# Performance work log

Measured on AMD Instinct MI355X. Metric: run time of the kernel, lower is better.

Reference implementation:

```python
import jax, jax.numpy as jnp
import numpy as np

IN_DIM = 128
HID = 128
OUT = 1
N_USER = 100000
N_ITEM = 50000
E = 1000000


def _mlp_params(key, in_dim, hid, out):
    k0, k1, k2 = jax.random.split(key, 3)
    s0 = float(np.sqrt(2.0 / in_dim))
    s1 = float(np.sqrt(2.0 / hid))
    return dict(
        W0=jax.random.normal(k0, (in_dim, hid), jnp.float32) * s0,
        b0=jnp.zeros((hid,), jnp.float32),
        W1=jax.random.normal(k1, (hid, hid), jnp.float32) * s1,
        b1=jnp.zeros((hid,), jnp.float32),
        W2=jax.random.normal(k2, (hid, out), jnp.float32) * s1,
        b2=jnp.zeros((out,), jnp.float32),
    )


def setup_inputs() -> dict:
    key = jax.random.key(0)
    ks = jax.random.split(key, 8)
    inp = {
        "user_emb": jax.random.normal(ks[0], (N_USER, IN_DIM), jnp.float32),
        "item_emb": jax.random.normal(ks[1], (N_ITEM, IN_DIM), jnp.float32),
        "ui_src": jax.random.randint(ks[2], (E,), 0, N_USER, jnp.int64),
        "ui_dst": jax.random.randint(ks[3], (E,), 0, N_ITEM, jnp.int64),
        "iu_src": jax.random.randint(ks[4], (E,), 0, N_ITEM, jnp.int64),
        "iu_dst": jax.random.randint(ks[5], (E,), 0, N_USER, jnp.int64),
    }
    for name, k in (("ui", ks[6]), ("iu", ks[7])):
        p = _mlp_params(k, 2 * IN_DIM, HID, OUT)
        for pn, pv in p.items():
            inp[f"{pn}_{name}"] = pv
    return inp


def _decode(src_emb, dst_emb, src_idx, dst_idx, W0, b0, W1, b1, W2, b2):
    # gather + concat -> [E, 2*in_dim]
    e = jnp.concatenate([src_emb[src_idx], dst_emb[dst_idx]], axis=1)
    h = jax.nn.elu(e @ W0 + b0)   # bilinear layer + ELU
    h = jax.nn.elu(h @ W1 + b1)   # linear1 + ELU
    return jax.nn.sigmoid(h @ W2 + b2).reshape(-1)  # linear2 + sigmoid, [E]


def reference(user_emb, item_emb, ui_src, ui_dst, iu_src, iu_dst,
              W0_ui, b0_ui, W1_ui, b1_ui, W2_ui, b2_ui,
              W0_iu, b0_iu, W1_iu, b1_iu, W2_iu, b2_iu):
    p_ui = _decode(user_emb, item_emb, ui_src, ui_dst,
                   W0_ui, b0_ui, W1_ui, b1_ui, W2_ui, b2_ui)
    p_iu = _decode(item_emb, user_emb, iu_src, iu_dst,
                   W0_iu, b0_iu, W1_iu, b1_iu, W2_iu, b2_iu)
    return p_ui, p_iu
```

## Files before the change

kernel.cpp:

```cpp
#include <hip/hip_runtime.h>
#include <cstdint>
#include <cstddef>


#define E_EDGES       1000000
#define NTILES        31250
#define GRID_BLKS     512
#define WAVES_PER_DEC 2048

typedef _Float16 half8  __attribute__((ext_vector_type(8)));
typedef _Float16 half4v __attribute__((ext_vector_type(4)));
typedef _Float16 half2v __attribute__((ext_vector_type(2)));
typedef float    f32x4  __attribute__((ext_vector_type(4)));
typedef unsigned int uint4v __attribute__((ext_vector_type(4)));

__device__ __forceinline__ float elu_f(float x) {
    return (x > 0.f) ? x : (__expf(x) - 1.f);
}

__device__ __forceinline__ void mfma_a(f32x4& acc, half8 af, half8 bf) {
    asm("v_mfma_f32_16x16x32_f16 %0, %1, %2, %0"
        : "+a"(acc)
        : "v"(af), "v"(bf));
}

__device__ __forceinline__ void xpose_pair(unsigned int A0, unsigned int A1,
                                           unsigned int& lo, unsigned int& hi) {
#if __has_builtin(__builtin_amdgcn_permlane32_swap) && __has_builtin(__builtin_amdgcn_permlane16_swap)
    auto t = __builtin_amdgcn_permlane32_swap(A0, A1, false, false);
    auto u = __builtin_amdgcn_permlane16_swap(t[0], t[1], false, false);
    lo = u[0]; hi = u[1];
#else
    const int l = (int)(threadIdx.x & 63);
    const int src = (((l >> 4) & 1) << 5) | (l & 15);
    unsigned int x0 = (unsigned int)__shfl((int)A0, src);
    unsigned int x1 = (unsigned int)__shfl((int)A1, src);
    unsigned int y0 = (unsigned int)__shfl((int)A0, src + 16);
    unsigned int y1 = (unsigned int)__shfl((int)A1, src + 16);
    lo = (l < 32) ? x0 : x1;
    hi = (l < 32) ? y0 : y1;
#endif
}

__global__ void cvt_tables(const float* __restrict__ u, const float* __restrict__ it,
                           _Float16* __restrict__ ou, _Float16* __restrict__ oi,
                           int n4u, int n4i) {
    int i = blockIdx.x * blockDim.x + threadIdx.x;
    const float4* src; half4v* dst; int j;
    if (i < n4u) { src = (const float4*)u; dst = (half4v*)ou; j = i; }
    else {
        j = i - n4u;
        if (j >= n4i) return;
        src = (const float4*)it; dst = (half4v*)oi;
    }
    float4 f = src[j];
    half4v h;
    h[0] = (_Float16)f.x; h[1] = (_Float16)f.y;
    h[2] = (_Float16)f.z; h[3] = (_Float16)f.w;
    dst[j] = h;
}

template<bool PRE16>
__global__ __launch_bounds__(512, 2) void edge_mlp(
    const void* __restrict__ tabU, const void* __restrict__ tabI,
    const int* __restrict__ ui_src, const int* __restrict__ ui_dst,
    const int* __restrict__ iu_src, const int* __restrict__ iu_dst,
    const float* __restrict__ W0_ui, const float* __restrict__ b0_ui,
    const float* __restrict__ W1_ui, const float* __restrict__ b1_ui,
    const float* __restrict__ W2_ui, const float* __restrict__ b2_ui,
    const float* __restrict__ W0_iu, const float* __restrict__ b0_iu,
    const float* __restrict__ W1_iu, const float* __restrict__ b1_iu,
    const float* __restrict__ W2_iu, const float* __restrict__ b2_iu,
    float* __restrict__ out)
{
    __shared__ __align__(16) _Float16 wlds[49152];

    const int dec = blockIdx.x & 1;
    const void* src_tab = dec ? tabI : tabU;
    const void* dst_tab = dec ? tabU : tabI;
    const int* src_idx = dec ? iu_src : ui_src;
    const int* dst_idx = dec ? iu_dst : ui_dst;
    const float* W0 = dec ? W0_iu : W0_ui;
    const float* b0 = dec ? b0_iu : b0_ui;
    const float* W1 = dec ? W1_iu : W1_ui;
    const float* b1 = dec ? b1_iu : b1_ui;
    const float* W2 = dec ? W2_iu : W2_ui;
    const float* b2 = dec ? b2_iu : b2_ui;
    float* op = out + (dec ? E_EDGES : 0);

    const int tid = threadIdx.x;
    const int l = tid & 63;
    const int w = tid >> 6;
    const int n = l & 15;
    const int g = l >> 4;

    #pragma unroll
    for (int q = 0; q < 8; ++q) {
        const int f = w * 8 + q;
        const int kk = f >> 3, hr = f & 7;
        const int kbase = kk * 32 + g * 8;
        const int col = hr * 16 + n;
        half8 fr;
        #pragma unroll
        for (int i = 0; i < 8; ++i) fr[i] = (_Float16)W0[(kbase + i) * 128 + col];
        *(half8*)&wlds[f * 512 + l * 8] = fr;
    }
    #pragma unroll
    for (int q = 0; q < 4; ++q) {
        const int f = w * 4 + q;
        const int kk = f >> 3, hr = f & 7;
        const int kbase = kk * 32 + g * 8;
        const int col = hr * 16 + n;
        half8 fr;
        #pragma unroll
        for (int i = 0; i < 8; ++i) fr[i] = (_Float16)W1[(kbase + i) * 128 + col];
        *(half8*)&wlds[32768 + f * 512 + l * 8] = fr;
    }

    f32x4 b0r[8], b1r[8], w2r[8];
    #pragma unroll
    for (int hr = 0; hr < 8; ++hr) {
        b0r[hr] = *(const f32x4*)&b0[hr * 16 + g * 4];
        b1r[hr] = *(const f32x4*)&b1[hr * 16 + g * 4];
        w2r[hr] = *(const f32x4*)&W2[hr * 16 + g * 4];
    }
    const float b2s = b2[0];
    __syncthreads();

    const half8* w0f = (const half8*)&wlds[0];
    const half8* w1f = (const half8*)&wlds[32768];

    const int wid = (blockIdx.x >> 1) * 8 + w;

    for (int t = wid; t < NTILES; t += WAVES_PER_DEC) {
        const int e0 = t * 32;

        half8 a[2][8];
        #pragma unroll
        for (int s = 0; s < 2; ++s) {
            const int e = e0 + s * 16 + n;
            const int si = src_idx[e];
            const int di = dst_idx[e];
            if constexpr (PRE16) {
                const half8* rs = (const half8*)((const _Float16*)src_tab + (size_t)si * 128) + g;
                const half8* rd = (const half8*)((const _Float16*)dst_tab + (size_t)di * 128) + g;
                #pragma unroll
                for (int kk = 0; kk < 4; ++kk) a[s][kk]     = rs[kk * 4];
                #pragma unroll
                for (int kk = 0; kk < 4; ++kk) a[s][4 + kk] = rd[kk * 4];
            } else {
                const float* rs = (const float*)src_tab + (size_t)si * 128 + g * 8;
                const float* rd = (const float*)dst_tab + (size_t)di * 128 + g * 8;
                #pragma unroll
                for (int kk = 0; kk < 8; ++kk) {
                    const float* base = (kk < 4) ? (rs + kk * 32) : (rd + (kk - 4) * 32);
                    float4 p0 = *(const float4*)base;
                    float4 p1 = *(const float4*)(base + 4);
                    half8 fr;
                    fr[0] = (_Float16)p0.x; fr[1] = (_Float16)p0.y;
                    fr[2] = (_Float16)p0.z; fr[3] = (_Float16)p0.w;
                    fr[4] = (_Float16)p1.x; fr[5] = (_Float16)p1.y;
                    fr[6] = (_Float16)p1.z; fr[7] = (_Float16)p1.w;
                    a[s][kk] = fr;
                }
            }
        }

        f32x4 acc0[2][8];
        #pragma unroll
        for (int s = 0; s < 2; ++s)
            #pragma unroll
            for (int hr = 0; hr < 8; ++hr) acc0[s][hr] = (f32x4){0.f, 0.f, 0.f, 0.f};
        #pragma unroll
        for (int kk = 0; kk < 8; ++kk) {
            #pragma unroll
            for (int hr = 0; hr < 8; ++hr) {
                const half8 wf = w0f[(kk * 8 + hr) * 64 + l];
                mfma_a(acc0[0][hr], wf, a[0][kk]);
                mfma_a(acc0[1][hr], wf, a[1][kk]);
            }
        }

        unsigned int v01[2][8], v23[2][8];
        #pragma unroll
        for (int hr = 0; hr < 8; ++hr) {
            #pragma unroll
            for (int s = 0; s < 2; ++s) {
                half2v p01, p23;
                p01[0] = (_Float16)elu_f(acc0[s][hr][0] + b0r[hr][0]);
                p01[1] = (_Float16)elu_f(acc0[s][hr][1] + b0r[hr][1]);
                p23[0] = (_Float16)elu_f(acc0[s][hr][2] + b0r[hr][2]);
                p23[1] = (_Float16)elu_f(acc0[s][hr][3] + b0r[hr][3]);
                v01[s][hr] = __builtin_bit_cast(unsigned int, p01);
                v23[s][hr] = __builtin_bit_cast(unsigned int, p23);
            }
        }
        half8 bfr[2][4];
        #pragma unroll
        for (int s = 0; s < 2; ++s) {
            #pragma unroll
            for (int kk = 0; kk < 4; ++kk) {
                unsigned int w0lo, w0hi, w1lo, w1hi;
                xpose_pair(v01[s][2 * kk], v01[s][2 * kk + 1], w0lo, w0hi);
                xpose_pair(v23[s][2 * kk], v23[s][2 * kk + 1], w1lo, w1hi);
                uint4v wd;
                wd.x = w0lo;
                wd.y = w1lo;
                wd.z = w0hi;
                wd.w = w1hi;
                bfr[s][kk] = __builtin_bit_cast(half8, wd);
            }
        }

        f32x4 acc1[2][8];
        #pragma unroll
        for (int s = 0; s < 2; ++s)
            #pragma unroll
            for (int hr = 0; hr < 8; ++hr) acc1[s][hr] = (f32x4){0.f, 0.f, 0.f, 0.f};
        #pragma unroll
        for (int kk = 0; kk < 4; ++kk) {
            #pragma unroll
            for (int hr = 0; hr < 8; ++hr) {
                const half8 wf = w1f[(kk * 8 + hr) * 64 + l];
                mfma_a(acc1[0][hr], wf, bfr[0][kk]);
                mfma_a(acc1[1][hr], wf, bfr[1][kk]);
            }
        }

        float accs0 = 0.f, accs1 = 0.f;
        #pragma unroll
        for (int hr = 0; hr < 8; ++hr) {
            #pragma unroll
            for (int v = 0; v < 4; ++v) {
                accs0 += elu_f(acc1[0][hr][v] + b1r[hr][v]) * w2r[hr][v];
                accs1 += elu_f(acc1[1][hr][v] + b1r[hr][v]) * w2r[hr][v];
            }
        }
        accs0 += __shfl_xor(accs0, 16); accs0 += __shfl_xor(accs0, 32);
        accs1 += __shfl_xor(accs1, 16); accs1 += __shfl_xor(accs1, 32);
        if (l < 32) {
            const float sel = (l & 16) ? accs1 : accs0;
            op[e0 + l] = 1.f / (1.f + __expf(-(sel + b2s)));
        }
    }
}

extern "C" void kernel_launch(void* const* d_in, const int* in_sizes, int n_in,
                              void* d_out, int out_size, void* d_ws, size_t ws_size,
                              hipStream_t stream) {
    const float* user_emb = (const float*)d_in[0];
    const float* item_emb = (const float*)d_in[1];
    const int* ui_src = (const int*)d_in[2];
    const int* ui_dst = (const int*)d_in[3];
    const int* iu_src = (const int*)d_in[4];
    const int* iu_dst = (const int*)d_in[5];
    const float* W0_ui = (const float*)d_in[6];
    const float* b0_ui = (const float*)d_in[7];
    const float* W1_ui = (const float*)d_in[8];
    const float* b1_ui = (const float*)d_in[9];
    const float* W2_ui = (const float*)d_in[10];
    const float* b2_ui = (const float*)d_in[11];
    const float* W0_iu = (const float*)d_in[12];
    const float* b0_iu = (const float*)d_in[13];
    const float* W1_iu = (const float*)d_in[14];
    const float* b1_iu = (const float*)d_in[15];
    const float* W2_iu = (const float*)d_in[16];
    const float* b2_iu = (const float*)d_in[17];
    float* out = (float*)d_out;

    const size_t nuser = (size_t)100000 * 128;
    const size_t nitem = (size_t)50000 * 128;
    const size_t need = (nuser + nitem) * sizeof(unsigned short);

    if (ws_size >= need) {
        _Float16* u16 = (_Float16*)d_ws;
        _Float16* i16 = u16 + nuser;
        const int n4u = (int)(nuser / 4);
        const int n4i = (int)(nitem / 4);
        cvt_tables<<<dim3((unsigned)((n4u + n4i + 255) / 256)), dim3(256), 0, stream>>>(
            user_emb, item_emb, u16, i16, n4u, n4i);
        edge_mlp<true><<<dim3(GRID_BLKS), dim3(512), 0, stream>>>(
            (const void*)u16, (const void*)i16,
            ui_src, ui_dst, iu_src, iu_dst,
            W0_ui, b0_ui, W1_ui, b1_ui, W2_ui, b2_ui,
            W0_iu, b0_iu, W1_iu, b1_iu, W2_iu, b2_iu, out);
    } else {
        edge_mlp<false><<<dim3(GRID_BLKS), dim3(512), 0, stream>>>(
            (const void*)user_emb, (const void*)item_emb,
            ui_src, ui_dst, iu_src, iu_dst,
            W0_ui, b0_ui, W1_ui, b1_ui, W2_ui, b2_ui,
            W0_iu, b0_iu, W1_iu, b1_iu, W2_iu, b2_iu, out);
    }
}
```

Measured before the change: 422.7 us.

## Software-pipeline embedding gathers and index loads across tiles in edge MLP loop

```diff
diff --git a/kernel.cpp b/kernel.cpp
--- a/kernel.cpp
+++ b/kernel.cpp
@@ -10,12 +10,15 @@
 
 typedef _Float16 half8  __attribute__((ext_vector_type(8)));
 typedef _Float16 half4v __attribute__((ext_vector_type(4)));
-typedef _Float16 half2v __attribute__((ext_vector_type(2)));
 typedef float    f32x4  __attribute__((ext_vector_type(4)));
 typedef unsigned int uint4v __attribute__((ext_vector_type(4)));
 
 __device__ __forceinline__ float elu_f(float x) {
     return (x > 0.f) ? x : (__expf(x) - 1.f);
+}
+
+__device__ __forceinline__ unsigned int pk16(float lo, float hi) {
+    return __builtin_bit_cast(unsigned int, __builtin_amdgcn_cvt_pkrtz(lo, hi));
 }
 
 __device__ __forceinline__ void mfma_a(f32x4& acc, half8 af, half8 bf) {
@@ -61,6 +64,51 @@
 }
 
 template<bool PRE16>
+__device__ __forceinline__ void gather_tiles(
+    half8 (&a)[2][8], const void* src_tab, const void* dst_tab,
+    const int (&si)[2], const int (&di)[2], int g)
+{
+    #pragma unroll
+    for (int s = 0; s < 2; ++s) {
+        if constexpr (PRE16) {
+            const half8* rs = (const half8*)((const _Float16*)src_tab + (size_t)si[s] * 128) + g;
+            const half8* rd = (const half8*)((const _Float16*)dst_tab + (size_t)di[s] * 128) + g;
+            #pragma unroll
+            for (int kk = 0; kk < 4; ++kk) a[s][kk]     = rs[kk * 4];
+            #pragma unroll
+            for (int kk = 0; kk < 4; ++kk) a[s][4 + kk] = rd[kk * 4];
+        } else {
+            const float* rs = (const float*)src_tab + (size_t)si[s] * 128 + g * 8;
+            const float* rd = (const float*)dst_tab + (size_t)di[s] * 128 + g * 8;
+            #pragma unroll
+            for (int kk = 0; kk < 8; ++kk) {
+                const float* base = (kk < 4) ? (rs + kk * 32) : (rd + (kk - 4) * 32);
+                float4 p0 = *(const float4*)base;
+                float4 p1 = *(const float4*)(base + 4);
+                half8 fr;
+                fr[0] = (_Float16)p0.x; fr[1] = (_Float16)p0.y;
+                fr[2] = (_Float16)p0.z; fr[3] = (_Float16)p0.w;
+                fr[4] = (_Float16)p1.x; fr[5] = (_Float16)p1.y;
+                fr[6] = (_Float16)p1.z; fr[7] = (_Float16)p1.w;
+                a[s][kk] = fr;
+            }
+        }
+    }
+}
+
+__device__ __forceinline__ void idx_load(const int* __restrict__ src_idx,
+                                         const int* __restrict__ dst_idx,
+                                         int t, int n, int (&si)[2], int (&di)[2])
+{
+    #pragma unroll
+    for (int s = 0; s < 2; ++s) {
+        const int e = t * 32 + s * 16 + n;
+        si[s] = src_idx[e];
+        di[s] = dst_idx[e];
+    }
+}
+
+template<bool PRE16>
 __global__ __launch_bounds__(512, 2) void edge_mlp(
     const void* __restrict__ tabU, const void* __restrict__ tabI,
     const int* __restrict__ ui_src, const int* __restrict__ ui_dst,
@@ -132,45 +180,20 @@
 
     const int wid = (blockIdx.x >> 1) * 8 + w;
 
-    for (int t = wid; t < NTILES; t += WAVES_PER_DEC) {
-        const int e0 = t * 32;
-
-        half8 a[2][8];
-        #pragma unroll
-        for (int s = 0; s < 2; ++s) {
-            const int e = e0 + s * 16 + n;
-            const int si = src_idx[e];
-            const int di = dst_idx[e];
-            if constexpr (PRE16) {
-                const half8* rs = (const half8*)((const _Float16*)src_tab + (size_t)si * 128) + g;
-                const half8* rd = (const half8*)((const _Float16*)dst_tab + (size_t)di * 128) + g;
-                #pragma unroll
-                for (int kk = 0; kk < 4; ++kk) a[s][kk]     = rs[kk * 4];
-                #pragma unroll
-                for (int kk = 0; kk < 4; ++kk) a[s][4 + kk] = rd[kk * 4];
-            } else {
-                const float* rs = (const float*)src_tab + (size_t)si * 128 + g * 8;
-                const float* rd = (const float*)dst_tab + (size_t)di * 128 + g * 8;
-                #pragma unroll
-                for (int kk = 0; kk < 8; ++kk) {
-                    const float* base = (kk < 4) ? (rs + kk * 32) : (rd + (kk - 4) * 32);
-                    float4 p0 = *(const float4*)base;
-                    float4 p1 = *(const float4*)(base + 4);
-                    half8 fr;
-                    fr[0] = (_Float16)p0.x; fr[1] = (_Float16)p0.y;
-                    fr[2] = (_Float16)p0.z; fr[3] = (_Float16)p0.w;
-                    fr[4] = (_Float16)p1.x; fr[5] = (_Float16)p1.y;
-                    fr[6] = (_Float16)p1.z; fr[7] = (_Float16)p1.w;
-                    a[s][kk] = fr;
-                }
-            }
-        }
-
+    int tc = wid;
+    int si[2], di[2];
+    idx_load(src_idx, dst_idx, tc, n, si, di);
+    half8 a[2][8];
+    gather_tiles<PRE16>(a, src_tab, dst_tab, si, di, g);
+    int tn = tc + WAVES_PER_DEC;
+    idx_load(src_idx, dst_idx, (tn < NTILES) ? tn : tc, n, si, di);
+
+    while (true) {
         f32x4 acc0[2][8];
         #pragma unroll
         for (int s = 0; s < 2; ++s)
             #pragma unroll
-            for (int hr = 0; hr < 8; ++hr) acc0[s][hr] = (f32x4){0.f, 0.f, 0.f, 0.f};
+            for (int hr = 0; hr < 8; ++hr) acc0[s][hr] = b0r[hr];
         #pragma unroll
         for (int kk = 0; kk < 8; ++kk) {
             #pragma unroll
@@ -181,18 +204,23 @@
             }
         }
 
+        __builtin_amdgcn_sched_barrier(0);
+
+        gather_tiles<PRE16>(a, src_tab, dst_tab, si, di, g);
+        {
+            const int tnc = (tn < NTILES) ? tn : tc;
+            const int t2 = tn + WAVES_PER_DEC;
+            const int t2c = (t2 < NTILES) ? t2 : tnc;
+            idx_load(src_idx, dst_idx, t2c, n, si, di);
+        }
+
         unsigned int v01[2][8], v23[2][8];
         #pragma unroll
         for (int hr = 0; hr < 8; ++hr) {
             #pragma unroll
             for (int s = 0; s < 2; ++s) {
-                half2v p01, p23;
-                p01[0] = (_Float16)elu_f(acc0[s][hr][0] + b0r[hr][0]);
-                p01[1] = (_Float16)elu_f(acc0[s][hr][1] + b0r[hr][1]);
-                p23[0] = (_Float16)elu_f(acc0[s][hr][2] + b0r[hr][2]);
-                p23[1] = (_Float16)elu_f(acc0[s][hr][3] + b0r[hr][3]);
-                v01[s][hr] = __builtin_bit_cast(unsigned int, p01);
-                v23[s][hr] = __builtin_bit_cast(unsigned int, p23);
+                v01[s][hr] = pk16(elu_f(acc0[s][hr][0]), elu_f(acc0[s][hr][1]));
+                v23[s][hr] = pk16(elu_f(acc0[s][hr][2]), elu_f(acc0[s][hr][3]));
             }
         }
         half8 bfr[2][4];
@@ -216,7 +244,7 @@
         #pragma unroll
         for (int s = 0; s < 2; ++s)
             #pragma unroll
-            for (int hr = 0; hr < 8; ++hr) acc1[s][hr] = (f32x4){0.f, 0.f, 0.f, 0.f};
+            for (int hr = 0; hr < 8; ++hr) acc1[s][hr] = b1r[hr];
         #pragma unroll
         for (int kk = 0; kk < 4; ++kk) {
             #pragma unroll
@@ -232,16 +260,20 @@
         for (int hr = 0; hr < 8; ++hr) {
             #pragma unroll
             for (int v = 0; v < 4; ++v) {
-                accs0 += elu_f(acc1[0][hr][v] + b1r[hr][v]) * w2r[hr][v];
-                accs1 += elu_f(acc1[1][hr][v] + b1r[hr][v]) * w2r[hr][v];
+                accs0 += elu_f(acc1[0][hr][v]) * w2r[hr][v];
+                accs1 += elu_f(acc1[1][hr][v]) * w2r[hr][v];
             }
         }
         accs0 += __shfl_xor(accs0, 16); accs0 += __shfl_xor(accs0, 32);
         accs1 += __shfl_xor(accs1, 16); accs1 += __shfl_xor(accs1, 32);
         if (l < 32) {
             const float sel = (l & 16) ? accs1 : accs0;
-            op[e0 + l] = 1.f / (1.f + __expf(-(sel + b2s)));
-        }
+            op[tc * 32 + l] = 1.f / (1.f + __expf(-(sel + b2s)));
+        }
+
+        if (tn >= NTILES) break;
+        tc = tn;
+        tn = tc + WAVES_PER_DEC;
     }
 }
 
```

Measured after the change: 380.4 us. -10.0%, faster.
